# Kernel tuning notes

Hardware: AMD Instinct MI355X
Metric: run time of the kernel (lower is better)

Reference implementation:

```python
import jax, jax.numpy as jnp
import numpy as np


def setup_inputs() -> dict:
    key = jax.random.key(0)
    k1, k2, k3 = jax.random.split(key, 3)
    B, Nin, Din, Nout, Dout = 32, 512, 64, 32, 64
    w_const = float(np.sqrt(Nout / (Din * Nin)))  # weight_init_const from module
    return {
        "input_pose": jax.random.normal(k1, (B, Nin, Din), dtype=jnp.float32),
        "current_act": jax.random.uniform(k2, (B, Nin), dtype=jnp.float32),
        "W": w_const * jax.random.normal(k3, (Nin, Din, Nout, Dout), dtype=jnp.float32),
        "num_iter": 3,
    }


def reference(input_pose, current_act, W, num_iter):
    # input_pose: [B, Nin, Din], current_act: [B, Nin], W: [Nin, Din, Nout, Dout]
    Nin, Din, Nout, Dout = W.shape
    scale = 1.0 / np.sqrt(Dout)

    # Vote projection is iteration-invariant: compute once.  [B, Nin, Nout, Dout]
    votes = jnp.einsum('bna,namd->bnmd', input_pose, W)

    # Initial pass: q0 = softmax(zeros) = uniform 1/Nout over classes.
    # einsum('nm,bna,namd->bmd', q0, pose, W) == votes.sum(n) / Nout
    next_capsule_value = votes.sum(axis=1) / Nout  # [B, Nout, Dout]

    query_key = None
    for _ in range(max(1, num_iter)):
        # 'bna,namd,bmd->bnm' == contraction of cached votes with current class poses
        logits = jnp.einsum('bnmd,bmd->bnm', votes, next_capsule_value) * scale
        query_key = jax.nn.softmax(logits, axis=2)  # [B, Nin, Nout]
        # 'bnm,bna,namd,bn->bmd' == activation-weighted vote aggregation
        next_capsule_value = jnp.einsum('bnm,bnmd,bn->bmd', query_key, votes, current_act)

    # act_type == 'EM' and next_act is None -> pose L2 norm
    next_act = jnp.linalg.norm(next_capsule_value, axis=-1)  # [B, Nout]

    # per-route x per-class interaction embeddings  [B, Nin, Nout, Dout]
    weights = query_key * current_act[..., None]
    route_class_emb = weights[..., None] * votes

    return next_capsule_value, next_act, query_key, route_class_emb
```

## Files before the change

### kernel.cpp

```cpp
#include <hip/hip_runtime.h>

#define B_    32
#define NIN   512
#define DIN   64
#define NOUT  32
#define DOUT  64
#define NUM_ITER 3

__global__ __launch_bounds__(256) void k_votes(const float* __restrict__ pose,
                                               const float* __restrict__ W,
                                               float* __restrict__ votes) {
    const int logical = (blockIdx.x & 7) * 256 + (blockIdx.x >> 3);
    const int n  = logical >> 2;
    const int b0 = (logical & 3) * 8;
    const int tid = threadIdx.x;
    const int m  = tid >> 3;
    const int d8 = tid & 7;

    __shared__ float poseL[8 * 64];
    if (tid < 128) {
        int bb = tid >> 4, a4 = tid & 15;
        float4 v = *((const float4*)(pose + (size_t)((b0 + bb) * NIN + n) * DIN) + a4);
        *(float4*)&poseL[bb * 64 + a4 * 4] = v;
    }
    __syncthreads();

    const float4* wp = (const float4*)W + (size_t)n * 32768 + m * 16 + d8 * 2;

    float4 acc0[8] = {};
    float4 acc1[8] = {};

#define CAP_STEP(AA, COMP)                                                  \
    {                                                                       \
        _Pragma("unroll")                                                   \
        for (int bb = 0; bb < 8; ++bb) {                                    \
            float p = pt[bb].COMP;                                          \
            acc0[bb].x = fmaf(p, wv[AA][0].x, acc0[bb].x);                  \
            acc0[bb].y = fmaf(p, wv[AA][0].y, acc0[bb].y);                  \
            acc0[bb].z = fmaf(p, wv[AA][0].z, acc0[bb].z);                  \
            acc0[bb].w = fmaf(p, wv[AA][0].w, acc0[bb].w);                  \
            acc1[bb].x = fmaf(p, wv[AA][1].x, acc1[bb].x);                  \
            acc1[bb].y = fmaf(p, wv[AA][1].y, acc1[bb].y);                  \
            acc1[bb].z = fmaf(p, wv[AA][1].z, acc1[bb].z);                  \
            acc1[bb].w = fmaf(p, wv[AA][1].w, acc1[bb].w);                  \
        }                                                                   \
    }

    for (int a0 = 0; a0 < 64; a0 += 4) {
        float4 wv[4][2];
#pragma unroll
        for (int aa = 0; aa < 4; ++aa) {
            wv[aa][0] = wp[(size_t)(a0 + aa) * 512];
            wv[aa][1] = wp[(size_t)(a0 + aa) * 512 + 1];
        }
        float4 pt[8];
#pragma unroll
        for (int bb = 0; bb < 8; ++bb)
            pt[bb] = *(const float4*)&poseL[bb * 64 + a0];

        CAP_STEP(0, x)
        CAP_STEP(1, y)
        CAP_STEP(2, z)
        CAP_STEP(3, w)
    }
#undef CAP_STEP

#pragma unroll
    for (int bb = 0; bb < 8; ++bb) {
        float4* vo = (float4*)votes +
                     ((size_t)((b0 + bb) * NIN + n)) * 512 + m * 16 + d8 * 2;
        vo[0] = acc0[bb];
        vo[1] = acc1[bb];
    }
}

__global__ __launch_bounds__(256) void k_ncv0(const float* __restrict__ votes,
                                              float* __restrict__ ncv) {
    int gid = blockIdx.x * 256 + threadIdx.x;
    int nc = gid >> 16;
    int e  = gid & 65535;
    int b  = e >> 11;
    int r  = e & 2047;
    const float* vp = votes + (size_t)b * (NIN * 2048) + (size_t)nc * 64 * 2048 + r;
    float s = 0.f;
#pragma unroll 8
    for (int nn = 0; nn < 64; ++nn) s += vp[nn * 2048];
    atomicAdd(&ncv[e], s * (1.0f / NOUT));
}

__global__ __launch_bounds__(256) void k_iter(float* __restrict__ votes,
                                              const float* __restrict__ act,
                                              const float* __restrict__ ncv_in,
                                              float* __restrict__ ncv_out,
                                              float* __restrict__ qk_out,
                                              int last) {
    const int b = blockIdx.x >> 5;
    const int chunk = blockIdx.x & 31;
    const int tid = threadIdx.x;
    const int wave = tid >> 6, lane = tid & 63;
    const int m = lane & 31, half = lane >> 5;
    const int sl = m * 64 + half * 32;

    const float4* np = (const float4*)(ncv_in + (size_t)b * 2048 + sl);
    float4 ncvs[8];
#pragma unroll
    for (int i = 0; i < 8; ++i) ncvs[i] = np[i];

    float4 acc[8];
#pragma unroll
    for (int i = 0; i < 8; ++i) acc[i] = make_float4(0.f, 0.f, 0.f, 0.f);

    const int n0 = chunk * 16 + wave * 4;

    for (int nn = 0; nn < 4; ++nn) {
        const int n = n0 + nn;
        float4* vp = (float4*)(votes + (size_t)(b * NIN + n) * 2048 + sl);
        float4 v[8];
#pragma unroll
        for (int i = 0; i < 8; ++i) v[i] = vp[i];

        float part = 0.f;
#pragma unroll
        for (int i = 0; i < 8; ++i) {
            part = fmaf(v[i].x, ncvs[i].x, part);
            part = fmaf(v[i].y, ncvs[i].y, part);
            part = fmaf(v[i].z, ncvs[i].z, part);
            part = fmaf(v[i].w, ncvs[i].w, part);
        }
        part += __shfl_xor(part, 32);
        float lg = part * 0.125f;

        float mx = lg;
#pragma unroll
        for (int off = 16; off >= 1; off >>= 1) mx = fmaxf(mx, __shfl_xor(mx, off));
        float e = __expf(lg - mx);
        float s = e;
#pragma unroll
        for (int off = 16; off >= 1; off >>= 1) s += __shfl_xor(s, off);
        float qk = e / s;
        if (half == 0) qk_out[(size_t)(b * NIN + n) * NOUT + m] = qk;

        const float qa = qk * act[b * NIN + n];
#pragma unroll
        for (int i = 0; i < 8; ++i) {
            acc[i].x = fmaf(qa, v[i].x, acc[i].x);
            acc[i].y = fmaf(qa, v[i].y, acc[i].y);
            acc[i].z = fmaf(qa, v[i].z, acc[i].z);
            acc[i].w = fmaf(qa, v[i].w, acc[i].w);
        }
        if (last) {
#pragma unroll
            for (int i = 0; i < 8; ++i) {
                float4 ev;
                ev.x = qa * v[i].x; ev.y = qa * v[i].y;
                ev.z = qa * v[i].z; ev.w = qa * v[i].w;
                vp[i] = ev;
            }
        }
    }

    __shared__ float accW[4][64 * 33];
    const int lid = m * 2 + half;
    float* aw = &accW[wave][lid * 33];
#pragma unroll
    for (int i = 0; i < 8; ++i) {
        aw[4 * i + 0] = acc[i].x; aw[4 * i + 1] = acc[i].y;
        aw[4 * i + 2] = acc[i].z; aw[4 * i + 3] = acc[i].w;
    }
    __syncthreads();
    for (int e = tid; e < 2048; e += 256) {
        int mm = e >> 6, dd = e & 63;
        int idx = (mm * 2 + (dd >> 5)) * 33 + (dd & 31);
        float s = accW[0][idx] + accW[1][idx] + accW[2][idx] + accW[3][idx];
        atomicAdd(&ncv_out[(size_t)b * 2048 + e], s);
    }
}

__global__ __launch_bounds__(256) void k_final_ncv(const float* __restrict__ ncv,
                                                   float* __restrict__ ncv_out,
                                                   float* __restrict__ act_out) {
    int gid = blockIdx.x * 256 + threadIdx.x;
    ncv_out[gid] = ncv[gid];
    if (gid < B_ * NOUT) {
        const float* p = ncv + gid * DOUT;
        float s = 0.f;
#pragma unroll 8
        for (int d = 0; d < DOUT; ++d) s = fmaf(p[d], p[d], s);
        act_out[gid] = sqrtf(s);
    }
}

extern "C" void kernel_launch(void* const* d_in, const int* in_sizes, int n_in,
                              void* d_out, int out_size, void* d_ws, size_t ws_size,
                              hipStream_t stream) {
    const float* pose = (const float*)d_in[0];
    const float* act  = (const float*)d_in[1];
    const float* W    = (const float*)d_in[2];

    float* out = (float*)d_out;
    float* ncv_out = out;
    float* act_out = out + 65536;
    float* qk_out  = out + 66560;
    float* emb_out = out + 590848;

    char* ws = (char*)d_ws;
    float* ncvA = (float*)ws;
    float* ncvB = (float*)(ws + 262144);

    float* votes = emb_out;

    k_votes<<<NIN * 4, 256, 0, stream>>>(pose, W, votes);

    hipMemsetAsync(ncvA, 0, B_ * NOUT * DOUT * sizeof(float), stream);
    k_ncv0<<<2048, 256, 0, stream>>>(votes, ncvA);

    float* cur = ncvA;
    float* nxt = ncvB;
    for (int it = 0; it < NUM_ITER; ++it) {
        hipMemsetAsync(nxt, 0, B_ * NOUT * DOUT * sizeof(float), stream);
        k_iter<<<B_ * 32, 256, 0, stream>>>(votes, act, cur, nxt, qk_out,
                                            it == NUM_ITER - 1 ? 1 : 0);
        float* t = cur; cur = nxt; nxt = t;
    }

    k_final_ncv<<<256, 256, 0, stream>>>(cur, ncv_out, act_out);
}
```

Before: 585.4 us.

## Fuse initial vote sum into vote kernel and replace atomics with deterministic partial reductions

The vote kernel now handles four input capsules per block and accumulates per-block partial sums of the votes. This removes the separate k_ncv0 pass that re-read the whole votes tensor. The iteration kernel writes per-chunk partials to a workspace instead of doing atomicAdd, and a small reduction kernel combines them, which also drops the memsets and the final copy/norm kernel. The iteration thread mapping now uses coalesced stride-64 float4 loads with shuffle reductions over 16-lane groups, and qk is written only on the last iteration. The cost is an extra 32MB partial buffer round trip and one more small kernel launch per iteration.

```diff
diff --git a/kernel.cpp b/kernel.cpp
--- a/kernel.cpp
+++ b/kernel.cpp
@@ -9,102 +9,108 @@
 
 __global__ __launch_bounds__(256) void k_votes(const float* __restrict__ pose,
                                                const float* __restrict__ W,
-                                               float* __restrict__ votes) {
-    const int logical = (blockIdx.x & 7) * 256 + (blockIdx.x >> 3);
-    const int n  = logical >> 2;
-    const int b0 = (logical & 3) * 8;
+                                               float* __restrict__ votes,
+                                               float* __restrict__ part0) {
+    const int bi = blockIdx.x;
+    const int nc = (bi >> 5) * 8 + (bi & 7);
+    const int bq = (bi >> 3) & 3;
+    const int b0 = bq * 8;
     const int tid = threadIdx.x;
     const int m  = tid >> 3;
     const int d8 = tid & 7;
 
-    __shared__ float poseL[8 * 64];
-    if (tid < 128) {
-        int bb = tid >> 4, a4 = tid & 15;
-        float4 v = *((const float4*)(pose + (size_t)((b0 + bb) * NIN + n) * DIN) + a4);
-        *(float4*)&poseL[bb * 64 + a4 * 4] = v;
+    __shared__ float poseL[4][8][64];
+#pragma unroll
+    for (int k = 0; k < 2; ++k) {
+        int j = tid + k * 256;
+        int nn = j >> 7, bb = (j >> 4) & 7, a4 = j & 15;
+        float4 v = *((const float4*)(pose +
+                     ((size_t)(b0 + bb) * NIN + nc * 4 + nn) * DIN) + a4);
+        *(float4*)&poseL[nn][bb][a4 * 4] = v;
     }
     __syncthreads();
 
-    const float4* wp = (const float4*)W + (size_t)n * 32768 + m * 16 + d8 * 2;
-
-    float4 acc0[8] = {};
-    float4 acc1[8] = {};
+    float4 nc0[8] = {}, nc1[8] = {};
 
 #define CAP_STEP(AA, COMP)                                                  \
     {                                                                       \
         _Pragma("unroll")                                                   \
         for (int bb = 0; bb < 8; ++bb) {                                    \
             float p = pt[bb].COMP;                                          \
-            acc0[bb].x = fmaf(p, wv[AA][0].x, acc0[bb].x);                  \
-            acc0[bb].y = fmaf(p, wv[AA][0].y, acc0[bb].y);                  \
-            acc0[bb].z = fmaf(p, wv[AA][0].z, acc0[bb].z);                  \
-            acc0[bb].w = fmaf(p, wv[AA][0].w, acc0[bb].w);                  \
-            acc1[bb].x = fmaf(p, wv[AA][1].x, acc1[bb].x);                  \
-            acc1[bb].y = fmaf(p, wv[AA][1].y, acc1[bb].y);                  \
-            acc1[bb].z = fmaf(p, wv[AA][1].z, acc1[bb].z);                  \
-            acc1[bb].w = fmaf(p, wv[AA][1].w, acc1[bb].w);                  \
+            a0[bb].x = fmaf(p, wv[AA][0].x, a0[bb].x);                      \
+            a0[bb].y = fmaf(p, wv[AA][0].y, a0[bb].y);                      \
+            a0[bb].z = fmaf(p, wv[AA][0].z, a0[bb].z);                      \
+            a0[bb].w = fmaf(p, wv[AA][0].w, a0[bb].w);                      \
+            a1[bb].x = fmaf(p, wv[AA][1].x, a1[bb].x);                      \
+            a1[bb].y = fmaf(p, wv[AA][1].y, a1[bb].y);                      \
+            a1[bb].z = fmaf(p, wv[AA][1].z, a1[bb].z);                      \
+            a1[bb].w = fmaf(p, wv[AA][1].w, a1[bb].w);                      \
         }                                                                   \
     }
 
-    for (int a0 = 0; a0 < 64; a0 += 4) {
-        float4 wv[4][2];
-#pragma unroll
-        for (int aa = 0; aa < 4; ++aa) {
-            wv[aa][0] = wp[(size_t)(a0 + aa) * 512];
-            wv[aa][1] = wp[(size_t)(a0 + aa) * 512 + 1];
-        }
-        float4 pt[8];
-#pragma unroll
-        for (int bb = 0; bb < 8; ++bb)
-            pt[bb] = *(const float4*)&poseL[bb * 64 + a0];
-
-        CAP_STEP(0, x)
-        CAP_STEP(1, y)
-        CAP_STEP(2, z)
-        CAP_STEP(3, w)
+    for (int nn = 0; nn < 4; ++nn) {
+        const int n = nc * 4 + nn;
+        const float4* wp = (const float4*)W + (size_t)n * 32768 + m * 16 + d8 * 2;
+        float4 a0[8] = {}, a1[8] = {};
+        for (int as = 0; as < 64; as += 4) {
+            float4 wv[4][2];
+#pragma unroll
+            for (int aa = 0; aa < 4; ++aa) {
+                wv[aa][0] = wp[(size_t)(as + aa) * 512];
+                wv[aa][1] = wp[(size_t)(as + aa) * 512 + 1];
+            }
+            float4 pt[8];
+#pragma unroll
+            for (int bb = 0; bb < 8; ++bb)
+                pt[bb] = *(const float4*)&poseL[nn][bb][as];
+            CAP_STEP(0, x)
+            CAP_STEP(1, y)
+            CAP_STEP(2, z)
+            CAP_STEP(3, w)
+        }
+#pragma unroll
+        for (int bb = 0; bb < 8; ++bb) {
+            float4* vo = (float4*)votes +
+                         ((size_t)(b0 + bb) * NIN + n) * 512 + m * 16 + d8 * 2;
+            vo[0] = a0[bb];
+            vo[1] = a1[bb];
+            nc0[bb].x += a0[bb].x; nc0[bb].y += a0[bb].y;
+            nc0[bb].z += a0[bb].z; nc0[bb].w += a0[bb].w;
+            nc1[bb].x += a1[bb].x; nc1[bb].y += a1[bb].y;
+            nc1[bb].z += a1[bb].z; nc1[bb].w += a1[bb].w;
+        }
     }
 #undef CAP_STEP
 
 #pragma unroll
     for (int bb = 0; bb < 8; ++bb) {
-        float4* vo = (float4*)votes +
-                     ((size_t)((b0 + bb) * NIN + n)) * 512 + m * 16 + d8 * 2;
-        vo[0] = acc0[bb];
-        vo[1] = acc1[bb];
-    }
-}
-
-__global__ __launch_bounds__(256) void k_ncv0(const float* __restrict__ votes,
-                                              float* __restrict__ ncv) {
-    int gid = blockIdx.x * 256 + threadIdx.x;
-    int nc = gid >> 16;
-    int e  = gid & 65535;
-    int b  = e >> 11;
-    int r  = e & 2047;
-    const float* vp = votes + (size_t)b * (NIN * 2048) + (size_t)nc * 64 * 2048 + r;
-    float s = 0.f;
-#pragma unroll 8
-    for (int nn = 0; nn < 64; ++nn) s += vp[nn * 2048];
-    atomicAdd(&ncv[e], s * (1.0f / NOUT));
+        float4* pp = (float4*)part0 +
+                     ((size_t)nc * 32 + (b0 + bb)) * 512 + m * 16 + d8 * 2;
+        pp[0] = nc0[bb];
+        pp[1] = nc1[bb];
+    }
 }
 
 __global__ __launch_bounds__(256) void k_iter(float* __restrict__ votes,
                                               const float* __restrict__ act,
                                               const float* __restrict__ ncv_in,
-                                              float* __restrict__ ncv_out,
+                                              float* __restrict__ part,
                                               float* __restrict__ qk_out,
                                               int last) {
     const int b = blockIdx.x >> 5;
     const int chunk = blockIdx.x & 31;
     const int tid = threadIdx.x;
     const int wave = tid >> 6, lane = tid & 63;
-    const int m = lane & 31, half = lane >> 5;
-    const int sl = m * 64 + half * 32;
-
-    const float4* np = (const float4*)(ncv_in + (size_t)b * 2048 + sl);
+    const int g = lane >> 4;
+
+    const float4* np = (const float4*)ncv_in + (size_t)b * 512 + lane;
     float4 ncvs[8];
 #pragma unroll
-    for (int i = 0; i < 8; ++i) ncvs[i] = np[i];
+    for (int i = 0; i < 8; ++i) {
+        float4 t = np[i * 64];
+        t.x *= 0.125f; t.y *= 0.125f; t.z *= 0.125f; t.w *= 0.125f;
+        ncvs[i] = t;
+    }
 
     float4 acc[8];
 #pragma unroll
@@ -114,79 +120,100 @@
 
     for (int nn = 0; nn < 4; ++nn) {
         const int n = n0 + nn;
-        float4* vp = (float4*)(votes + (size_t)(b * NIN + n) * 2048 + sl);
+        float4* vp = (float4*)votes + (size_t)(b * NIN + n) * 512 + lane;
         float4 v[8];
 #pragma unroll
-        for (int i = 0; i < 8; ++i) v[i] = vp[i];
-
-        float part = 0.f;
+        for (int i = 0; i < 8; ++i) v[i] = vp[i * 64];
+
+        float sc[8];
 #pragma unroll
         for (int i = 0; i < 8; ++i) {
-            part = fmaf(v[i].x, ncvs[i].x, part);
-            part = fmaf(v[i].y, ncvs[i].y, part);
-            part = fmaf(v[i].z, ncvs[i].z, part);
-            part = fmaf(v[i].w, ncvs[i].w, part);
-        }
-        part += __shfl_xor(part, 32);
-        float lg = part * 0.125f;
-
-        float mx = lg;
-#pragma unroll
-        for (int off = 16; off >= 1; off >>= 1) mx = fmaxf(mx, __shfl_xor(mx, off));
-        float e = __expf(lg - mx);
-        float s = e;
-#pragma unroll
-        for (int off = 16; off >= 1; off >>= 1) s += __shfl_xor(s, off);
-        float qk = e / s;
-        if (half == 0) qk_out[(size_t)(b * NIN + n) * NOUT + m] = qk;
-
-        const float qa = qk * act[b * NIN + n];
-#pragma unroll
-        for (int i = 0; i < 8; ++i) {
-            acc[i].x = fmaf(qa, v[i].x, acc[i].x);
-            acc[i].y = fmaf(qa, v[i].y, acc[i].y);
-            acc[i].z = fmaf(qa, v[i].z, acc[i].z);
-            acc[i].w = fmaf(qa, v[i].w, acc[i].w);
-        }
+            float p = v[i].x * ncvs[i].x;
+            p = fmaf(v[i].y, ncvs[i].y, p);
+            p = fmaf(v[i].z, ncvs[i].z, p);
+            p = fmaf(v[i].w, ncvs[i].w, p);
+            sc[i] = p;
+        }
+#pragma unroll
+        for (int off = 1; off <= 8; off <<= 1) {
+#pragma unroll
+            for (int i = 0; i < 8; ++i) sc[i] += __shfl_xor(sc[i], off);
+        }
+        float mx = sc[0];
+#pragma unroll
+        for (int i = 1; i < 8; ++i) mx = fmaxf(mx, sc[i]);
+        mx = fmaxf(mx, __shfl_xor(mx, 16));
+        mx = fmaxf(mx, __shfl_xor(mx, 32));
+        float e[8], ss = 0.f;
+#pragma unroll
+        for (int i = 0; i < 8; ++i) { e[i] = __expf(sc[i] - mx); ss += e[i]; }
+        ss += __shfl_xor(ss, 16);
+        ss += __shfl_xor(ss, 32);
+        const float inv = 1.0f / ss;
+        const float an = act[b * NIN + n];
+
         if (last) {
+            if ((lane & 15) == 0) {
+#pragma unroll
+                for (int i = 0; i < 8; ++i)
+                    qk_out[(size_t)(b * NIN + n) * NOUT + i * 4 + g] = e[i] * inv;
+            }
 #pragma unroll
             for (int i = 0; i < 8; ++i) {
-                float4 ev;
-                ev.x = qa * v[i].x; ev.y = qa * v[i].y;
-                ev.z = qa * v[i].z; ev.w = qa * v[i].w;
-                vp[i] = ev;
-            }
-        }
-    }
-
-    __shared__ float accW[4][64 * 33];
-    const int lid = m * 2 + half;
-    float* aw = &accW[wave][lid * 33];
-#pragma unroll
-    for (int i = 0; i < 8; ++i) {
-        aw[4 * i + 0] = acc[i].x; aw[4 * i + 1] = acc[i].y;
-        aw[4 * i + 2] = acc[i].z; aw[4 * i + 3] = acc[i].w;
-    }
+                const float qa = e[i] * inv * an;
+                float4 t;
+                t.x = qa * v[i].x; t.y = qa * v[i].y;
+                t.z = qa * v[i].z; t.w = qa * v[i].w;
+                acc[i].x += t.x; acc[i].y += t.y;
+                acc[i].z += t.z; acc[i].w += t.w;
+                vp[i * 64] = t;
+            }
+        } else {
+#pragma unroll
+            for (int i = 0; i < 8; ++i) {
+                const float qa = e[i] * inv * an;
+                acc[i].x = fmaf(qa, v[i].x, acc[i].x);
+                acc[i].y = fmaf(qa, v[i].y, acc[i].y);
+                acc[i].z = fmaf(qa, v[i].z, acc[i].z);
+                acc[i].w = fmaf(qa, v[i].w, acc[i].w);
+            }
+        }
+    }
+
+    __shared__ float4 accL[4][512];
+#pragma unroll
+    for (int i = 0; i < 8; ++i) accL[wave][i * 64 + lane] = acc[i];
     __syncthreads();
-    for (int e = tid; e < 2048; e += 256) {
-        int mm = e >> 6, dd = e & 63;
-        int idx = (mm * 2 + (dd >> 5)) * 33 + (dd & 31);
-        float s = accW[0][idx] + accW[1][idx] + accW[2][idx] + accW[3][idx];
-        atomicAdd(&ncv_out[(size_t)b * 2048 + e], s);
-    }
-}
-
-__global__ __launch_bounds__(256) void k_final_ncv(const float* __restrict__ ncv,
-                                                   float* __restrict__ ncv_out,
-                                                   float* __restrict__ act_out) {
-    int gid = blockIdx.x * 256 + threadIdx.x;
-    ncv_out[gid] = ncv[gid];
-    if (gid < B_ * NOUT) {
-        const float* p = ncv + gid * DOUT;
-        float s = 0.f;
-#pragma unroll 8
-        for (int d = 0; d < DOUT; ++d) s = fmaf(p[d], p[d], s);
-        act_out[gid] = sqrtf(s);
+    for (int j = tid; j < 512; j += 256) {
+        float4 s = accL[0][j];
+        float4 t1 = accL[1][j], t2 = accL[2][j], t3 = accL[3][j];
+        s.x += t1.x + t2.x + t3.x;
+        s.y += t1.y + t2.y + t3.y;
+        s.z += t1.z + t2.z + t3.z;
+        s.w += t1.w + t2.w + t3.w;
+        ((float4*)part)[((size_t)chunk * 32 + b) * 512 + j] = s;
+    }
+}
+
+__global__ __launch_bounds__(256) void k_red(const float4* __restrict__ src,
+                                             float* __restrict__ dst,
+                                             int nchunks, float scale,
+                                             float* __restrict__ act_out) {
+    const int gid = blockIdx.x * 256 + threadIdx.x;
+    const int b = gid >> 9, j = gid & 511;
+    float4 s = make_float4(0.f, 0.f, 0.f, 0.f);
+#pragma unroll 4
+    for (int c = 0; c < nchunks; ++c) {
+        float4 t = src[((size_t)c * 32 + b) * 512 + j];
+        s.x += t.x; s.y += t.y; s.z += t.z; s.w += t.w;
+    }
+    s.x *= scale; s.y *= scale; s.z *= scale; s.w *= scale;
+    ((float4*)dst)[(size_t)b * 512 + j] = s;
+    if (act_out) {
+        float ss = s.x * s.x + s.y * s.y + s.z * s.z + s.w * s.w;
+#pragma unroll
+        for (int off = 1; off <= 8; off <<= 1) ss += __shfl_xor(ss, off);
+        if ((j & 15) == 0) act_out[b * NOUT + (j >> 4)] = sqrtf(ss);
     }
 }
 
@@ -204,24 +231,22 @@
     float* emb_out = out + 590848;
 
     char* ws = (char*)d_ws;
-    float* ncvA = (float*)ws;
-    float* ncvB = (float*)(ws + 262144);
+    float* part = (float*)ws;
+    float* ncvA = (float*)(ws + 33554432);
+    float* ncvB = ncvA + 65536;
 
     float* votes = emb_out;
 
-    k_votes<<<NIN * 4, 256, 0, stream>>>(pose, W, votes);
-
-    hipMemsetAsync(ncvA, 0, B_ * NOUT * DOUT * sizeof(float), stream);
-    k_ncv0<<<2048, 256, 0, stream>>>(votes, ncvA);
-
-    float* cur = ncvA;
-    float* nxt = ncvB;
-    for (int it = 0; it < NUM_ITER; ++it) {
-        hipMemsetAsync(nxt, 0, B_ * NOUT * DOUT * sizeof(float), stream);
-        k_iter<<<B_ * 32, 256, 0, stream>>>(votes, act, cur, nxt, qk_out,
-                                            it == NUM_ITER - 1 ? 1 : 0);
-        float* t = cur; cur = nxt; nxt = t;
-    }
-
-    k_final_ncv<<<256, 256, 0, stream>>>(cur, ncv_out, act_out);
-}
+    k_votes<<<512, 256, 0, stream>>>(pose, W, votes, part);
+    k_red<<<64, 256, 0, stream>>>((const float4*)part, ncvA, 128,
+                                  1.0f / NOUT, nullptr);
+
+    k_iter<<<B_ * 32, 256, 0, stream>>>(votes, act, ncvA, part, qk_out, 0);
+    k_red<<<64, 256, 0, stream>>>((const float4*)part, ncvB, 32, 1.0f, nullptr);
+
+    k_iter<<<B_ * 32, 256, 0, stream>>>(votes, act, ncvB, part, qk_out, 0);
+    k_red<<<64, 256, 0, stream>>>((const float4*)part, ncvA, 32, 1.0f, nullptr);
+
+    k_iter<<<B_ * 32, 256, 0, stream>>>(votes, act, ncvA, part, qk_out, 1);
+    k_red<<<64, 256, 0, stream>>>((const float4*)part, ncv_out, 32, 1.0f, act_out);
+}
```

New measurement: 569.2 us. 1.03x faster.
